# Optimization experiments

Hardware: AMD Instinct MI355X
Metric: run time of the kernel (lower is better)

The kernel has to match this reference:

```python
import jax, jax.numpy as jnp
import numpy as np

B, C_IN, C_INTER, H, W_DIM = 8, 512, 256, 64, 64


def setup_inputs() -> dict:
    key = jax.random.key(0)
    k1, k2, k3, k4 = jax.random.split(key, 4)
    x = jax.random.normal(k1, (B, C_IN, H, W_DIM), dtype=jnp.float32)
    pem_feats = jax.random.normal(k2, (B, C_INTER, H * W_DIM), dtype=jnp.float32)
    # 1x1 conv weight stored as [out, in] (kernel spatial dims are 1x1)
    W = jax.random.normal(k3, (C_INTER, C_IN), dtype=jnp.float32) * (1.0 / np.sqrt(C_IN))
    bias = jax.random.normal(k4, (C_INTER,), dtype=jnp.float32) * 0.01
    return {"x": x, "pem_feats": pem_feats, "W": W, "bias": bias}


def reference(x, pem_feats, W, bias):
    b, c, h, w = x.shape
    # 1x1 conv == channel-mixing GEMM: [b, inter, h, w]
    proj = jnp.einsum('bchw,oc->bohw', x, W) + bias[None, :, None, None]
    proj = proj.reshape(b, -1, h * w)                      # [b, inter, hw]
    # weights[b,i,j] = <proj[:, i], pem[:, j]>  -> [b, hw, hw], softmax over j
    scores = jnp.einsum('bci,bcj->bij', proj, pem_feats)
    weights = jax.nn.softmax(scores, axis=-1)
    # out[b,k,i] = sum_j weights[b,j,i] * pem[b,k,j]
    eam = jnp.einsum('bji,bkj->bki', weights, pem_feats)   # [b, inter, hw]
    return eam.reshape(b, -1, h, w)
```

## Files before the change

### kernel.cpp

```cpp
#include <hip/hip_runtime.h>
#include <math.h>

#define BATCH 8
#define CIN 512
#define CO 256
#define HW 4096
#define KT 32
#define NSEG 4
#define SEGC 32

typedef unsigned short ushort_t;
typedef unsigned int uint_t;
typedef _Float16 v8h __attribute__((ext_vector_type(8)));
typedef _Float16 v4h __attribute__((ext_vector_type(4)));
typedef float v4f __attribute__((ext_vector_type(4)));
typedef float v16f __attribute__((ext_vector_type(16)));
typedef ushort_t u16x8 __attribute__((ext_vector_type(8)));

__device__ __forceinline__ ushort_t f2h(float f) {
  return __builtin_bit_cast(ushort_t, (_Float16)f);
}
__device__ __forceinline__ v4f mfma16h(v8h a, v8h b, v4f c) {
  return __builtin_amdgcn_mfma_f32_16x16x32_f16(a, b, c, 0, 0, 0);
}
__device__ __forceinline__ v16f mfma32h(v8h a, v8h b, v16f c) {
  return __builtin_amdgcn_mfma_f32_32x32x16_f16(a, b, c, 0, 0, 0);
}
__device__ __forceinline__ v8h lds_frag_h512(const unsigned char* base, int row, int cb) {
  uint4 v = *(const uint4*)(base + row * 512 + (((cb) ^ (row & 7)) << 4));
  return __builtin_bit_cast(v8h, v);
}
__device__ __forceinline__ v8h lds_frag_h128(const unsigned char* base, int row, int cb) {
  uint4 v = *(const uint4*)(base + row * 128 + (((cb) ^ (row & 7)) << 4));
  return __builtin_bit_cast(v8h, v);
}
__device__ __forceinline__ void gll16(const void* g, void* l) {
  __builtin_amdgcn_global_load_lds(
      (const __attribute__((address_space(1))) unsigned int*)g,
      (__attribute__((address_space(3))) unsigned int*)l, 16, 0, 0);
}
#define VMEM_BAR() do {                                            \
    asm volatile("s_waitcnt vmcnt(0) lgkmcnt(0)" ::: "memory");    \
    __builtin_amdgcn_sched_barrier(0);                             \
    __builtin_amdgcn_s_barrier();                                  \
    __builtin_amdgcn_sched_barrier(0);                             \
  } while (0)
#define LDS_BAR() do {                                             \
    asm volatile("s_waitcnt lgkmcnt(0)" ::: "memory");             \
    __builtin_amdgcn_sched_barrier(0);                             \
    __builtin_amdgcn_s_barrier();                                  \
    __builtin_amdgcn_sched_barrier(0);                             \
  } while (0)

__global__ __launch_bounds__(256) void k_w(
    const float* __restrict__ W, ushort_t* __restrict__ w_h) {
  int idx = blockIdx.x * 256 + threadIdx.x;
  size_t off = (size_t)idx * 8;
  float4 v0 = *(const float4*)&W[off];
  float4 v1 = *(const float4*)&W[off + 4];
  float f[8] = {v0.x, v0.y, v0.z, v0.w, v1.x, v1.y, v1.z, v1.w};
  u16x8 h;
#pragma unroll
  for (int j = 0; j < 8; ++j) h[j] = f2h(f[j]);
  *(u16x8*)&w_h[off] = h;
}

__global__ __launch_bounds__(256) void k_tr_x(
    const float* __restrict__ x, ushort_t* __restrict__ xt_h) {
  __shared__ float T[64][65];
  const int i0 = blockIdx.x * 64;
  const int c0 = blockIdx.y * 64;
  const int b  = blockIdx.z;
  const int t  = threadIdx.x;
  const int cl = t >> 4;
  const int i4 = (t & 15) * 4;
#pragma unroll
  for (int r = 0; r < 4; ++r) {
    int c = c0 + r * 16 + cl;
    size_t off = ((size_t)b * CIN + c) * HW + i0 + i4;
    float4 v = *(const float4*)&x[off];
    T[r * 16 + cl][i4 + 0] = v.x;
    T[r * 16 + cl][i4 + 1] = v.y;
    T[r * 16 + cl][i4 + 2] = v.z;
    T[r * 16 + cl][i4 + 3] = v.w;
  }
  __syncthreads();
  {
    int il = t >> 2;
    int cs = (t & 3) * 16;
    u16x8 h0, h1;
#pragma unroll
    for (int j = 0; j < 8; ++j) h0[j] = f2h(T[cs + j][il]);
#pragma unroll
    for (int j = 0; j < 8; ++j) h1[j] = f2h(T[cs + 8 + j][il]);
    size_t ro = ((size_t)b * HW + i0 + il) * CIN + c0 + cs;
    *(u16x8*)&xt_h[ro]     = h0;
    *(u16x8*)&xt_h[ro + 8] = h1;
  }
}

__global__ __launch_bounds__(256, 2) void k_proj_mfma(
    const ushort_t* __restrict__ xt_h, const ushort_t* __restrict__ w_h,
    const float* __restrict__ bias, ushort_t* __restrict__ proj_h) {
  __shared__ __align__(16) unsigned char L[2][128 * 128];
  const int bid = blockIdx.x;
  const int b = bid & 7;
  const int rest = bid >> 3;
  const int xt = rest & 31;
  const int oh = rest >> 5;
  const int x0 = xt * 128;
  const int t = threadIdx.x;
  const int lane = t & 63, wave = t >> 6;

  v4f acc[2][8];
#pragma unroll
  for (int xf = 0; xf < 2; ++xf)
#pragma unroll
    for (int of = 0; of < 8; ++of) acc[xf][of] = (v4f){0.f, 0.f, 0.f, 0.f};

  float bias_of[8];
#pragma unroll
  for (int of = 0; of < 8; ++of)
    bias_of[of] = bias[oh * 128 + of * 16 + (lane & 15)];

  for (int ch = 0; ch < 8; ++ch) {
    const int c0 = ch * 64;
#pragma unroll
    for (int i = 0; i < 4; ++i) {
      int G = i * 256 + t;
      int r = G >> 3, sl = G & 7;
      int cg = (sl ^ (r & 7)) << 3;
      size_t xsrc = ((size_t)b * HW + x0 + r) * CIN + c0 + cg;
      size_t wsrc = ((size_t)(oh * 128 + r)) * CIN + c0 + cg;
      unsigned lb = (unsigned)((i * 256 + wave * 64) << 4);
      gll16(&xt_h[xsrc], &L[0][lb]);
      gll16(&w_h[wsrc],  &L[1][lb]);
    }
    __syncthreads();
#pragma unroll
    for (int st = 0; st < 2; ++st) {
      int cb = st * 4 + (lane >> 4);
      v8h ah0 = lds_frag_h128(L[0], wave * 32 + (lane & 15), cb);
      v8h ah1 = lds_frag_h128(L[0], wave * 32 + 16 + (lane & 15), cb);
#pragma unroll
      for (int of = 0; of < 8; ++of) {
        v8h bh = lds_frag_h128(L[1], of * 16 + (lane & 15), cb);
        acc[0][of] = mfma16h(ah0, bh, acc[0][of]);
        acc[1][of] = mfma16h(ah1, bh, acc[1][of]);
      }
    }
    __syncthreads();
  }

  ushort_t* Th = (ushort_t*)&L[0][0];
#pragma unroll
  for (int xf = 0; xf < 2; ++xf)
#pragma unroll
    for (int of = 0; of < 8; ++of)
#pragma unroll
      for (int r = 0; r < 4; ++r) {
        int x_loc = wave * 32 + xf * 16 + (lane >> 4) * 4 + r;
        int o_loc = of * 16 + (lane & 15);
        Th[x_loc * 128 + o_loc] = f2h(acc[xf][of][r] + bias_of[of]);
      }
  __syncthreads();
  {
    int row = t >> 1, half = t & 1;
    size_t off = ((size_t)b * HW + x0 + row) * CO + oh * 128 + half * 64;
#pragma unroll
    for (int j = 0; j < 8; ++j)
      *(uint4*)&proj_h[off + j * 8] =
          *(const uint4*)&Th[row * 128 + half * 64 + j * 8];
  }
}

__global__ __launch_bounds__(256) void k_tr_pem(
    const float* __restrict__ pem,
    ushort_t* __restrict__ pem_t_h, ushort_t* __restrict__ pem_h) {
  __shared__ float T[64][65];
  const int y0 = blockIdx.x * 64;
  const int c0 = blockIdx.y * 64;
  const int b  = blockIdx.z;
  const int t  = threadIdx.x;
  const int cl = t >> 4;
  const int y4 = (t & 15) * 4;
#pragma unroll
  for (int r = 0; r < 4; ++r) {
    int c = c0 + r * 16 + cl;
    size_t off = ((size_t)b * CO + c) * HW + y0 + y4;
    float4 v = *(const float4*)&pem[off];
    ushort4 h;
    h.x = f2h(v.x); h.y = f2h(v.y); h.z = f2h(v.z); h.w = f2h(v.w);
    *(ushort4*)&pem_h[off] = h;
    T[r * 16 + cl][y4 + 0] = v.x;
    T[r * 16 + cl][y4 + 1] = v.y;
    T[r * 16 + cl][y4 + 2] = v.z;
    T[r * 16 + cl][y4 + 3] = v.w;
  }
  __syncthreads();
  {
    int yl = t >> 2;
    int cs = (t & 3) * 16;
    u16x8 h0, h1;
#pragma unroll
    for (int j = 0; j < 8; ++j) h0[j] = f2h(T[cs + j][yl]);
#pragma unroll
    for (int j = 0; j < 8; ++j) h1[j] = f2h(T[cs + 8 + j][yl]);
    size_t ro = ((size_t)b * HW + y0 + yl) * CO + c0 + cs;
    *(u16x8*)&pem_t_h[ro]     = h0;
    *(u16x8*)&pem_t_h[ro + 8] = h1;
  }
}

__global__ __launch_bounds__(512, 2) void k_stats_f16(
    const ushort_t* __restrict__ proj_h, const ushort_t* __restrict__ pem_t_h,
    float* __restrict__ m_seg, float* __restrict__ d_seg) {
  __shared__ __align__(16) unsigned char pbuf[2][32 * 512];
  const int id = blockIdx.x;
  const int b = id & 7;
  const int rest = id >> 3;
  const int xt = rest & 7;
  const int seg = rest >> 3;
  const int x0 = xt * 512;
  const int t = threadIdx.x;
  const int lane = t & 63, wave = t >> 6;
  const int xw = x0 + wave * 64;

  v8h Ah[4][8];
#pragma unroll
  for (int xf = 0; xf < 4; ++xf) {
    const size_t ro =
        ((size_t)b * HW + xw + xf * 16 + (lane & 15)) * CO + (lane >> 4) * 8;
#pragma unroll
    for (int st = 0; st < 8; ++st)
      Ah[xf][st] = __builtin_bit_cast(v8h, *(const uint4*)&proj_h[ro + st * 32]);
  }

  float m[4][4], d[4][4];
#pragma unroll
  for (int xf = 0; xf < 4; ++xf)
#pragma unroll
    for (int r = 0; r < 4; ++r) { m[xf][r] = -3.0e38f; d[xf][r] = 0.f; }

  auto stage = [&](int bufi, int tt) {
    const int yy0 = tt * 32;
#pragma unroll
    for (int i = 0; i < 2; ++i) {
      int G = i * 512 + t;
      int r = G >> 5, sl = G & 31;
      size_t so = ((size_t)b * HW + yy0 + r) * CO + ((sl ^ (r & 7)) << 3);
      unsigned lb = (unsigned)((i * 512 + wave * 64) << 4);
      gll16(&pem_t_h[so], &pbuf[bufi][lb]);
    }
  };

  const int tt0 = seg * SEGC;
  stage(0, tt0);
  __syncthreads();

  for (int tc = 0; tc < SEGC; ++tc) {
    if (tc + 1 < SEGC) stage((tc + 1) & 1, tt0 + tc + 1);

    const unsigned char* bp = pbuf[tc & 1];
    v4f acc[4][2];
#pragma unroll
    for (int xf = 0; xf < 4; ++xf)
#pragma unroll
      for (int yc = 0; yc < 2; ++yc) acc[xf][yc] = (v4f){0.f, 0.f, 0.f, 0.f};

#pragma unroll
    for (int st = 0; st < 8; ++st) {
#pragma unroll
      for (int yc = 0; yc < 2; ++yc) {
        v8h bh = lds_frag_h512(bp, yc * 16 + (lane & 15), st * 4 + (lane >> 4));
        acc[0][yc] = mfma16h(Ah[0][st], bh, acc[0][yc]);
        acc[1][yc] = mfma16h(Ah[1][st], bh, acc[1][yc]);
        acc[2][yc] = mfma16h(Ah[2][st], bh, acc[2][yc]);
        acc[3][yc] = mfma16h(Ah[3][st], bh, acc[3][yc]);
      }
    }

#pragma unroll
    for (int xf = 0; xf < 4; ++xf) {
      float mx8 = fmaxf(fmaxf(fmaxf(acc[xf][0][0], acc[xf][0][1]),
                              fmaxf(acc[xf][0][2], acc[xf][0][3])),
                        fmaxf(fmaxf(acc[xf][1][0], acc[xf][1][1]),
                              fmaxf(acc[xf][1][2], acc[xf][1][3])));
      float minm = fminf(fminf(m[xf][0], m[xf][1]), fminf(m[xf][2], m[xf][3]));
      if (__any(mx8 > minm + 8.0f)) {
#pragma unroll
        for (int r = 0; r < 4; ++r) {
          float rm = fmaxf(acc[xf][0][r], acc[xf][1][r]);
          rm = fmaxf(rm, __shfl_xor(rm, 1));
          rm = fmaxf(rm, __shfl_xor(rm, 2));
          rm = fmaxf(rm, __shfl_xor(rm, 4));
          rm = fmaxf(rm, __shfl_xor(rm, 8));
          float mn = fmaxf(m[xf][r], rm);
          d[xf][r] *= __expf(m[xf][r] - mn);
          m[xf][r] = mn;
        }
      }
#pragma unroll
      for (int r = 0; r < 4; ++r)
        d[xf][r] += __expf(acc[xf][0][r] - m[xf][r]) +
                    __expf(acc[xf][1][r] - m[xf][r]);
    }
    __syncthreads();
  }

#pragma unroll
  for (int xf = 0; xf < 4; ++xf) {
    float dv[4];
#pragma unroll
    for (int r = 0; r < 4; ++r) {
      float v = d[xf][r];
      v += __shfl_xor(v, 1);
      v += __shfl_xor(v, 2);
      v += __shfl_xor(v, 4);
      v += __shfl_xor(v, 8);
      dv[r] = v;
    }
    if ((lane & 15) == 0) {
      size_t o = ((size_t)(b * NSEG + seg)) * HW + xw + xf * 16 + (lane >> 4) * 4;
      *(float4*)&m_seg[o] = make_float4(m[xf][0], m[xf][1], m[xf][2], m[xf][3]);
      *(float4*)&d_seg[o] = make_float4(dv[0], dv[1], dv[2], dv[3]);
    }
  }
}

__global__ __launch_bounds__(256) void k_red2(
    const float* __restrict__ m_seg, const float* __restrict__ d_seg,
    float* __restrict__ Cx) {
  int idx = blockIdx.x * 256 + threadIdx.x;
  int b = idx >> 12;
  int xx = idx & 4095;
  float ms[NSEG], ds[NSEG];
  float mm = -3.0e38f;
#pragma unroll
  for (int s = 0; s < NSEG; ++s) {
    ms[s] = m_seg[((size_t)(b * NSEG + s)) * HW + xx];
    ds[s] = d_seg[((size_t)(b * NSEG + s)) * HW + xx];
    mm = fmaxf(mm, ms[s]);
  }
  float dd = 0.f;
#pragma unroll
  for (int s = 0; s < NSEG; ++s) dd += ds[s] * __expf(ms[s] - mm);
  Cx[(size_t)b * HW + xx] = mm + __logf(dd);
}

__global__ __launch_bounds__(512, 2) void k_fused(
    const ushort_t* __restrict__ proj_h, const ushort_t* __restrict__ pem_t_h,
    const ushort_t* __restrict__ pem_h, const float* __restrict__ Cx,
    float* __restrict__ out) {
  __shared__ __align__(16) unsigned char Lp[2][64 * 512];
  __shared__ __align__(16) unsigned char Lk[2][256 * 128];
  __shared__ __align__(16) unsigned char Le[128 * 128];
  const int id = blockIdx.x;
  const int b = id & 7;
  const int yt = id >> 3;
  const int y0 = yt * 128;
  const int t = threadIdx.x;
  const int lane = t & 63, wave = t >> 6;
  const int l31 = lane & 31, lh = lane >> 5;
  const int wx = wave & 1, wy = wave >> 1;
  const int kq = wave & 3, yq = wave >> 2;

  v8h Bres[16];
  {
    const size_t ro =
        ((size_t)b * HW + y0 + wy * 32 + l31) * CO + lh * 8;
#pragma unroll
    for (int st = 0; st < 16; ++st)
      Bres[st] = __builtin_bit_cast(v8h, *(const uint4*)&pem_t_h[ro + st * 16]);
  }

  v16f pv[2][2];
#pragma unroll
  for (int kt = 0; kt < 2; ++kt)
#pragma unroll
    for (int yy = 0; yy < 2; ++yy)
#pragma unroll
      for (int r = 0; r < 16; ++r) pv[kt][yy][r] = 0.f;

  auto stage = [&](int bufi, int xt) {
    const int x0s = xt * 64;
#pragma unroll
    for (int i = 0; i < 4; ++i) {
      int G = i * 512 + t;
      int r = G >> 5, sl = G & 31;
      size_t so = ((size_t)b * HW + x0s + r) * CO + ((sl ^ (r & 7)) << 3);
      gll16(&proj_h[so], &Lp[bufi][(unsigned)((i * 512 + wave * 64) << 4)]);
    }
#pragma unroll
    for (int i = 0; i < 4; ++i) {
      int G = i * 512 + t;
      int r = G >> 3, sl = G & 7;
      size_t so = ((size_t)b * CO + r) * HW + x0s + ((sl ^ (r & 7)) << 3);
      gll16(&pem_h[so], &Lk[bufi][(unsigned)((i * 512 + wave * 64) << 4)]);
    }
  };

  stage(0, 0);

  for (int xt = 0; xt < 64; ++xt) {
    const int cur = xt & 1;
    const int x0 = xt * 64;
    VMEM_BAR();

    float4 c4[4];
#pragma unroll
    for (int q = 0; q < 4; ++q)
      c4[q] = *(const float4*)&Cx[(size_t)b * HW + x0 + wx * 32 + 8 * q + 4 * lh];

    if (xt + 1 < 64) stage(cur ^ 1, xt + 1);

    v16f s;
#pragma unroll
    for (int r = 0; r < 16; ++r) s[r] = 0.f;
    __builtin_amdgcn_s_setprio(1);
#pragma unroll
    for (int st = 0; st < 16; ++st) {
      v8h a = lds_frag_h512(Lp[cur], wx * 32 + l31, st * 2 + lh);
      s = mfma32h(a, Bres[st], s);
    }
    __builtin_amdgcn_s_setprio(0);

    {
      int erow = wy * 32 + l31;
#pragma unroll
      for (int q = 0; q < 4; ++q) {
        float cc[4] = {c4[q].x, c4[q].y, c4[q].z, c4[q].w};
        v4h p;
#pragma unroll
        for (int r = 0; r < 4; ++r)
          p[r] = (_Float16)__expf(s[4 * q + r] - cc[r]);
        int gx = wx * 4 + q;
        *(uint2*)(Le + erow * 128 + ((gx ^ (erow & 7)) << 4) + lh * 8) =
            __builtin_bit_cast(uint2, p);
      }
    }
    LDS_BAR();

    __builtin_amdgcn_s_setprio(1);
#pragma unroll
    for (int st = 0; st < 4; ++st) {
      int cb = st * 2 + lh;
      v8h e0 = lds_frag_h128(Le, yq * 64 + l31, cb);
      v8h e1 = lds_frag_h128(Le, yq * 64 + 32 + l31, cb);
      v8h a0 = lds_frag_h128(Lk[cur], kq * 64 + l31, cb);
      v8h a1 = lds_frag_h128(Lk[cur], kq * 64 + 32 + l31, cb);
      pv[0][0] = mfma32h(a0, e0, pv[0][0]);
      pv[0][1] = mfma32h(a0, e1, pv[0][1]);
      pv[1][0] = mfma32h(a1, e0, pv[1][0]);
      pv[1][1] = mfma32h(a1, e1, pv[1][1]);
    }
    __builtin_amdgcn_s_setprio(0);
  }

#pragma unroll
  for (int kt = 0; kt < 2; ++kt)
#pragma unroll
    for (int yy = 0; yy < 2; ++yy)
#pragma unroll
      for (int r = 0; r < 16; ++r) {
        int k = kq * 64 + kt * 32 + (r & 3) + 8 * (r >> 2) + 4 * lh;
        int y = y0 + yq * 64 + yy * 32 + l31;
        out[((size_t)b * CO + k) * HW + y] = pv[kt][yy][r];
      }
}

__global__ __launch_bounds__(256) void k_proj(
    const float* __restrict__ x, const float* __restrict__ W,
    const float* __restrict__ bias, float* __restrict__ proj) {
  __shared__ float As[KT][68];
  __shared__ float Bs[KT][68];
  const int i0 = blockIdx.x * 64;
  const int o0 = blockIdx.y * 64;
  const int b  = blockIdx.z;
  const int t  = threadIdx.x;
  const int tx = t & 15, ty = t >> 4;
  const float* xb = x + (size_t)b * CIN * HW;
  float acc[4][4] = {};
  for (int c0 = 0; c0 < CIN; c0 += KT) {
#pragma unroll
    for (int l = 0; l < 8; ++l) {
      int idx = t + l * 256;
      int o = idx >> 5;
      int c = idx & 31;
      As[c][o] = W[(size_t)(o0 + o) * CIN + c0 + c];
    }
#pragma unroll
    for (int l = 0; l < 2; ++l) {
      int idx4 = t + l * 256;
      int c = idx4 >> 4;
      int i4 = idx4 & 15;
      *(float4*)&Bs[c][i4 * 4] =
          *(const float4*)&xb[(size_t)(c0 + c) * HW + i0 + i4 * 4];
    }
    __syncthreads();
#pragma unroll
    for (int c = 0; c < KT; ++c) {
      float4 a  = *(const float4*)&As[c][tx * 4];
      float4 bv = *(const float4*)&Bs[c][ty * 4];
      float av[4] = {a.x, a.y, a.z, a.w};
      float bb[4] = {bv.x, bv.y, bv.z, bv.w};
#pragma unroll
      for (int u = 0; u < 4; ++u)
#pragma unroll
        for (int v = 0; v < 4; ++v) acc[u][v] += av[u] * bb[v];
    }
    __syncthreads();
  }
  float* pbout = proj + (size_t)b * CO * HW;
#pragma unroll
  for (int u = 0; u < 4; ++u) {
    int o = o0 + tx * 4 + u;
    float bsv = bias[o];
    float4 r;
    r.x = acc[u][0] + bsv; r.y = acc[u][1] + bsv;
    r.z = acc[u][2] + bsv; r.w = acc[u][3] + bsv;
    *(float4*)&pbout[(size_t)o * HW + i0 + ty * 4] = r;
  }
}

__global__ __launch_bounds__(256) void k_stats(
    const float* __restrict__ proj, const float* __restrict__ pem,
    float* __restrict__ Mx, float* __restrict__ Dinv) {
  __shared__ float As[KT][68];
  __shared__ float Bs[KT][68];
  __shared__ float MsS[64][17];
  __shared__ float DsS[64][17];
  const int x0 = blockIdx.x * 64;
  const int b  = blockIdx.y;
  const int t  = threadIdx.x;
  const int tx = t & 15, ty = t >> 4;
  const float* pj = proj + (size_t)b * CO * HW;
  const float* pe = pem + (size_t)b * CO * HW;
  float m[4], d[4];
#pragma unroll
  for (int u = 0; u < 4; ++u) { m[u] = -3.0e38f; d[u] = 0.f; }
  for (int y0 = 0; y0 < HW; y0 += 64) {
    float s[4][4] = {};
    for (int c0 = 0; c0 < CO; c0 += KT) {
#pragma unroll
      for (int l = 0; l < 2; ++l) {
        int idx4 = t + l * 256;
        int c = idx4 >> 4, w4 = idx4 & 15;
        *(float4*)&As[c][w4 * 4] =
            *(const float4*)&pj[(size_t)(c0 + c) * HW + x0 + w4 * 4];
        *(float4*)&Bs[c][w4 * 4] =
            *(const float4*)&pe[(size_t)(c0 + c) * HW + y0 + w4 * 4];
      }
      __syncthreads();
#pragma unroll
      for (int c = 0; c < KT; ++c) {
        float4 a  = *(const float4*)&As[c][tx * 4];
        float4 bv = *(const float4*)&Bs[c][ty * 4];
        float av[4] = {a.x, a.y, a.z, a.w};
        float bb[4] = {bv.x, bv.y, bv.z, bv.w};
#pragma unroll
        for (int u = 0; u < 4; ++u)
#pragma unroll
          for (int v = 0; v < 4; ++v) s[u][v] += av[u] * bb[v];
      }
      __syncthreads();
    }
#pragma unroll
    for (int u = 0; u < 4; ++u) {
      float mv = fmaxf(fmaxf(s[u][0], s[u][1]), fmaxf(s[u][2], s[u][3]));
      if (mv > m[u]) { d[u] *= __expf(m[u] - mv); m[u] = mv; }
      d[u] += __expf(s[u][0] - m[u]) + __expf(s[u][1] - m[u]) +
              __expf(s[u][2] - m[u]) + __expf(s[u][3] - m[u]);
    }
  }
#pragma unroll
  for (int u = 0; u < 4; ++u) { MsS[tx * 4 + u][ty] = m[u]; DsS[tx * 4 + u][ty] = d[u]; }
  __syncthreads();
  if (t < 64) {
    float mm = -3.0e38f;
#pragma unroll
    for (int i = 0; i < 16; ++i) mm = fmaxf(mm, MsS[t][i]);
    float dd = 0.f;
#pragma unroll
    for (int i = 0; i < 16; ++i) dd += DsS[t][i] * __expf(MsS[t][i] - mm);
    Mx[(size_t)b * HW + x0 + t]   = mm;
    Dinv[(size_t)b * HW + x0 + t] = 1.0f / dd;
  }
}

__global__ __launch_bounds__(256) void k_out(
    const float* __restrict__ proj, const float* __restrict__ pem,
    const float* __restrict__ Mx, const float* __restrict__ Dinv,
    float* __restrict__ out) {
  __shared__ float As[KT][68];
  __shared__ float Bs[KT][68];
  __shared__ float E[64][68];
  const int y0 = blockIdx.x * 64;
  const int b  = blockIdx.y;
  const int t  = threadIdx.x;
  const int tx = t & 15, ty = t >> 4;
  const int kg = t >> 3, yg = t & 7;
  const float* pj = proj + (size_t)b * CO * HW;
  const float* pe = pem + (size_t)b * CO * HW;
  const float* Mb = Mx + (size_t)b * HW;
  const float* Db = Dinv + (size_t)b * HW;
  float acc[8][8] = {};
  for (int x0 = 0; x0 < HW; x0 += 64) {
    float s[4][4] = {};
    for (int c0 = 0; c0 < CO; c0 += KT) {
#pragma unroll
      for (int l = 0; l < 2; ++l) {
        int idx4 = t + l * 256;
        int c = idx4 >> 4, w4 = idx4 & 15;
        *(float4*)&As[c][w4 * 4] =
            *(const float4*)&pj[(size_t)(c0 + c) * HW + x0 + w4 * 4];
        *(float4*)&Bs[c][w4 * 4] =
            *(const float4*)&pe[(size_t)(c0 + c) * HW + y0 + w4 * 4];
      }
      __syncthreads();
#pragma unroll
      for (int c = 0; c < KT; ++c) {
        float4 a  = *(const float4*)&As[c][tx * 4];
        float4 bv = *(const float4*)&Bs[c][ty * 4];
        float av[4] = {a.x, a.y, a.z, a.w};
        float bb[4] = {bv.x, bv.y, bv.z, bv.w};
#pragma unroll
        for (int u = 0; u < 4; ++u)
#pragma unroll
          for (int v = 0; v < 4; ++v) s[u][v] += av[u] * bb[v];
      }
      __syncthreads();
    }
#pragma unroll
    for (int u = 0; u < 4; ++u) {
      int xr = x0 + tx * 4 + u;
      float mm = Mb[xr];
      float di = Db[xr];
      E[tx * 4 + u][ty * 4 + 0] = __expf(s[u][0] - mm) * di;
      E[tx * 4 + u][ty * 4 + 1] = __expf(s[u][1] - mm) * di;
      E[tx * 4 + u][ty * 4 + 2] = __expf(s[u][2] - mm) * di;
      E[tx * 4 + u][ty * 4 + 3] = __expf(s[u][3] - mm) * di;
    }
    __syncthreads();
    for (int xi = 0; xi < 64; xi += 4) {
      float4 p[8];
#pragma unroll
      for (int u = 0; u < 8; ++u)
        p[u] = *(const float4*)&pe[(size_t)(kg * 8 + u) * HW + x0 + xi];
#pragma unroll
      for (int j = 0; j < 4; ++j) {
        float4 e0 = *(const float4*)&E[xi + j][yg * 8];
        float4 e1 = *(const float4*)&E[xi + j][yg * 8 + 4];
        float evv[8] = {e0.x, e0.y, e0.z, e0.w, e1.x, e1.y, e1.z, e1.w};
#pragma unroll
        for (int u = 0; u < 8; ++u) {
          float a = (j == 0) ? p[u].x : (j == 1) ? p[u].y : (j == 2) ? p[u].z : p[u].w;
#pragma unroll
          for (int v = 0; v < 8; ++v) acc[u][v] += a * evv[v];
        }
      }
    }
    __syncthreads();
  }
#pragma unroll
  for (int u = 0; u < 8; ++u) {
    int k = kg * 8 + u;
    float4 r0, r1;
    r0.x = acc[u][0]; r0.y = acc[u][1]; r0.z = acc[u][2]; r0.w = acc[u][3];
    r1.x = acc[u][4]; r1.y = acc[u][5]; r1.z = acc[u][6]; r1.w = acc[u][7];
    float* ob = out + ((size_t)b * CO + k) * HW + y0 + yg * 8;
    *(float4*)&ob[0] = r0;
    *(float4*)&ob[4] = r1;
  }
}

extern "C" void kernel_launch(void* const* d_in, const int* in_sizes, int n_in,
                              void* d_out, int out_size, void* d_ws, size_t ws_size,
                              hipStream_t stream) {
  const float* x    = (const float*)d_in[0];
  const float* pem  = (const float*)d_in[1];
  const float* W    = (const float*)d_in[2];
  const float* bias = (const float*)d_in[3];
  float* out = (float*)d_out;

  const size_t NS   = (size_t)BATCH * HW * CO;
  const size_t NS2  = (size_t)BATCH * HW * CIN;
  const size_t HWB  = (size_t)BATCH * HW;
  const size_t SEGN = (size_t)BATCH * NSEG * HW;
  const size_t WN   = (size_t)CO * CIN;

  unsigned char* basep = (unsigned char*)d_ws;
  ushort_t* proj_h   = (ushort_t*)basep;
  ushort_t* pem_t_h  = proj_h + NS;
  ushort_t* pem_h    = pem_t_h + NS;
  float*    Cxp      = (float*)(pem_h + NS);
  float*    m_seg    = Cxp + HWB;
  float*    d_seg    = m_seg + SEGN;
  ushort_t* xt_h     = (ushort_t*)(d_seg + SEGN);
  ushort_t* w_h      = xt_h + NS2;

  const size_t need = 3 * NS * 2 + HWB * 4 + 2 * SEGN * 4 + NS2 * 2 + WN * 2;

  if (ws_size < need) {
    float* proj = (float*)d_ws;
    float* Mx2  = proj + NS;
    float* Di2  = Mx2 + HWB;
    const size_t need_f = (NS + 2 * HWB) * sizeof(float);
    if (ws_size < need_f) return;
    k_proj <<<dim3(HW / 64, CO / 64, BATCH), 256, 0, stream>>>(x, W, bias, proj);
    k_stats<<<dim3(HW / 64, BATCH),          256, 0, stream>>>(proj, pem, Mx2, Di2);
    k_out  <<<dim3(HW / 64, BATCH),          256, 0, stream>>>(proj, pem, Mx2, Di2, out);
    return;
  }

  k_w<<<64, 256, 0, stream>>>(W, w_h);
  k_tr_x<<<dim3(HW / 64, CIN / 64, BATCH), 256, 0, stream>>>(x, xt_h);
  k_proj_mfma<<<512, 256, 0, stream>>>(xt_h, w_h, bias, proj_h);
  k_tr_pem<<<dim3(HW / 64, CO / 64, BATCH), 256, 0, stream>>>(pem, pem_t_h, pem_h);

  k_stats_f16<<<256, 512, 0, stream>>>(proj_h, pem_t_h, m_seg, d_seg);
  k_red2<<<128, 256, 0, stream>>>(m_seg, d_seg, Cxp);
  k_fused<<<256, 512, 0, stream>>>(proj_h, pem_t_h, pem_h, Cxp, out);
}
```

Measured before the change: 313.2 us.

## Load GEMM operands directly from global memory and widen x-tile to 128

```diff
diff --git a/kernel.cpp b/kernel.cpp
--- a/kernel.cpp
+++ b/kernel.cpp
@@ -34,17 +34,18 @@
   uint4 v = *(const uint4*)(base + row * 128 + (((cb) ^ (row & 7)) << 4));
   return __builtin_bit_cast(v8h, v);
 }
+__device__ __forceinline__ v8h lds_frag_h256(const unsigned char* base, int row, int cb) {
+  uint4 v = *(const uint4*)(base + row * 256 + (((cb) ^ (row & 15)) << 4));
+  return __builtin_bit_cast(v8h, v);
+}
+__device__ __forceinline__ v8h gfrag(const ushort_t* p) {
+  return __builtin_bit_cast(v8h, *(const uint4*)p);
+}
 __device__ __forceinline__ void gll16(const void* g, void* l) {
   __builtin_amdgcn_global_load_lds(
       (const __attribute__((address_space(1))) unsigned int*)g,
       (__attribute__((address_space(3))) unsigned int*)l, 16, 0, 0);
 }
-#define VMEM_BAR() do {                                            \
-    asm volatile("s_waitcnt vmcnt(0) lgkmcnt(0)" ::: "memory");    \
-    __builtin_amdgcn_sched_barrier(0);                             \
-    __builtin_amdgcn_s_barrier();                                  \
-    __builtin_amdgcn_sched_barrier(0);                             \
-  } while (0)
 #define LDS_BAR() do {                                             \
     asm volatile("s_waitcnt lgkmcnt(0)" ::: "memory");             \
     __builtin_amdgcn_sched_barrier(0);                             \
@@ -352,9 +353,7 @@
     const ushort_t* __restrict__ proj_h, const ushort_t* __restrict__ pem_t_h,
     const ushort_t* __restrict__ pem_h, const float* __restrict__ Cx,
     float* __restrict__ out) {
-  __shared__ __align__(16) unsigned char Lp[2][64 * 512];
-  __shared__ __align__(16) unsigned char Lk[2][256 * 128];
-  __shared__ __align__(16) unsigned char Le[128 * 128];
+  __shared__ __align__(16) unsigned char Le[128 * 256];
   const int id = blockIdx.x;
   const int b = id & 7;
   const int yt = id >> 3;
@@ -362,13 +361,12 @@
   const int t = threadIdx.x;
   const int lane = t & 63, wave = t >> 6;
   const int l31 = lane & 31, lh = lane >> 5;
-  const int wx = wave & 1, wy = wave >> 1;
+  const int wxp = wave & 1, wy = wave >> 1;
   const int kq = wave & 3, yq = wave >> 2;
 
   v8h Bres[16];
   {
-    const size_t ro =
-        ((size_t)b * HW + y0 + wy * 32 + l31) * CO + lh * 8;
+    const size_t ro = ((size_t)b * HW + y0 + wy * 32 + l31) * CO + lh * 8;
 #pragma unroll
     for (int st = 0; st < 16; ++st)
       Bres[st] = __builtin_bit_cast(v8h, *(const uint4*)&pem_t_h[ro + st * 16]);
@@ -382,79 +380,77 @@
 #pragma unroll
       for (int r = 0; r < 16; ++r) pv[kt][yy][r] = 0.f;
 
-  auto stage = [&](int bufi, int xt) {
-    const int x0s = xt * 64;
-#pragma unroll
-    for (int i = 0; i < 4; ++i) {
-      int G = i * 512 + t;
-      int r = G >> 5, sl = G & 31;
-      size_t so = ((size_t)b * HW + x0s + r) * CO + ((sl ^ (r & 7)) << 3);
-      gll16(&proj_h[so], &Lp[bufi][(unsigned)((i * 512 + wave * 64) << 4)]);
-    }
-#pragma unroll
-    for (int i = 0; i < 4; ++i) {
-      int G = i * 512 + t;
-      int r = G >> 3, sl = G & 7;
-      size_t so = ((size_t)b * CO + r) * HW + x0s + ((sl ^ (r & 7)) << 3);
-      gll16(&pem_h[so], &Lk[bufi][(unsigned)((i * 512 + wave * 64) << 4)]);
-    }
-  };
-
-  stage(0, 0);
-
-  for (int xt = 0; xt < 64; ++xt) {
-    const int cur = xt & 1;
-    const int x0 = xt * 64;
-    VMEM_BAR();
-
-    float4 c4[4];
-#pragma unroll
-    for (int q = 0; q < 4; ++q)
-      c4[q] = *(const float4*)&Cx[(size_t)b * HW + x0 + wx * 32 + 8 * q + 4 * lh];
-
-    if (xt + 1 < 64) stage(cur ^ 1, xt + 1);
-
-    v16f s;
-#pragma unroll
-    for (int r = 0; r < 16; ++r) s[r] = 0.f;
-    __builtin_amdgcn_s_setprio(1);
-#pragma unroll
-    for (int st = 0; st < 16; ++st) {
-      v8h a = lds_frag_h512(Lp[cur], wx * 32 + l31, st * 2 + lh);
-      s = mfma32h(a, Bres[st], s);
-    }
-    __builtin_amdgcn_s_setprio(0);
+  const ushort_t* paS0 = proj_h + ((size_t)b * HW + (wxp * 2 + 0) * 32 + l31) * CO + lh * 8;
+  const ushort_t* paS1 = proj_h + ((size_t)b * HW + (wxp * 2 + 1) * 32 + l31) * CO + lh * 8;
+  const ushort_t* paP0 = pem_h + ((size_t)b * CO + kq * 64 + l31) * HW + lh * 8;
+  const ushort_t* paP1 = pem_h + ((size_t)b * CO + kq * 64 + 32 + l31) * HW + lh * 8;
+  const float* cxb = Cx + (size_t)b * HW;
+
+  for (int xt = 0; xt < 32; ++xt) {
+    const int x0 = xt * 128;
+
+    float4 c4[2][4];
+#pragma unroll
+    for (int xi = 0; xi < 2; ++xi)
+#pragma unroll
+      for (int q = 0; q < 4; ++q)
+        c4[xi][q] = *(const float4*)&cxb[x0 + (wxp * 2 + xi) * 32 + 8 * q + 4 * lh];
+
+    v16f s0, s1;
+#pragma unroll
+    for (int r = 0; r < 16; ++r) { s0[r] = 0.f; s1[r] = 0.f; }
+    {
+      const ushort_t* a0 = paS0 + (size_t)x0 * CO;
+      const ushort_t* a1 = paS1 + (size_t)x0 * CO;
+      __builtin_amdgcn_s_setprio(1);
+#pragma unroll
+      for (int st = 0; st < 16; ++st) {
+        s0 = mfma32h(gfrag(a0 + st * 16), Bres[st], s0);
+        s1 = mfma32h(gfrag(a1 + st * 16), Bres[st], s1);
+      }
+      __builtin_amdgcn_s_setprio(0);
+    }
 
     {
       int erow = wy * 32 + l31;
 #pragma unroll
-      for (int q = 0; q < 4; ++q) {
-        float cc[4] = {c4[q].x, c4[q].y, c4[q].z, c4[q].w};
-        v4h p;
-#pragma unroll
-        for (int r = 0; r < 4; ++r)
-          p[r] = (_Float16)__expf(s[4 * q + r] - cc[r]);
-        int gx = wx * 4 + q;
-        *(uint2*)(Le + erow * 128 + ((gx ^ (erow & 7)) << 4) + lh * 8) =
-            __builtin_bit_cast(uint2, p);
+      for (int xi = 0; xi < 2; ++xi) {
+#pragma unroll
+        for (int q = 0; q < 4; ++q) {
+          float cc[4] = {c4[xi][q].x, c4[xi][q].y, c4[xi][q].z, c4[xi][q].w};
+          v4h p;
+#pragma unroll
+          for (int r = 0; r < 4; ++r) {
+            float sv = (xi == 0) ? s0[4 * q + r] : s1[4 * q + r];
+            p[r] = (_Float16)__expf(sv - cc[r]);
+          }
+          int gx = (wxp * 2 + xi) * 4 + q;
+          *(uint2*)(Le + erow * 256 + ((gx ^ (erow & 15)) << 4) + lh * 8) =
+              __builtin_bit_cast(uint2, p);
+        }
       }
     }
     LDS_BAR();
 
-    __builtin_amdgcn_s_setprio(1);
-#pragma unroll
-    for (int st = 0; st < 4; ++st) {
-      int cb = st * 2 + lh;
-      v8h e0 = lds_frag_h128(Le, yq * 64 + l31, cb);
-      v8h e1 = lds_frag_h128(Le, yq * 64 + 32 + l31, cb);
-      v8h a0 = lds_frag_h128(Lk[cur], kq * 64 + l31, cb);
-      v8h a1 = lds_frag_h128(Lk[cur], kq * 64 + 32 + l31, cb);
-      pv[0][0] = mfma32h(a0, e0, pv[0][0]);
-      pv[0][1] = mfma32h(a0, e1, pv[0][1]);
-      pv[1][0] = mfma32h(a1, e0, pv[1][0]);
-      pv[1][1] = mfma32h(a1, e1, pv[1][1]);
-    }
-    __builtin_amdgcn_s_setprio(0);
+    {
+      const ushort_t* a0 = paP0 + x0;
+      const ushort_t* a1 = paP1 + x0;
+      __builtin_amdgcn_s_setprio(1);
+#pragma unroll
+      for (int st = 0; st < 8; ++st) {
+        int cb = st * 2 + lh;
+        v8h e0 = lds_frag_h256(Le, yq * 64 + l31, cb);
+        v8h e1 = lds_frag_h256(Le, yq * 64 + 32 + l31, cb);
+        v8h f0 = gfrag(a0 + st * 16);
+        v8h f1 = gfrag(a1 + st * 16);
+        pv[0][0] = mfma32h(f0, e0, pv[0][0]);
+        pv[0][1] = mfma32h(f0, e1, pv[0][1]);
+        pv[1][0] = mfma32h(f1, e0, pv[1][0]);
+        pv[1][1] = mfma32h(f1, e1, pv[1][1]);
+      }
+      __builtin_amdgcn_s_setprio(0);
+    }
+    LDS_BAR();
   }
 
 #pragma unroll
```

Result: slower. 565.1 us (+80.4%).
